# Kernel tuning notes

Measured on AMD Instinct MI355X. Metric: run time of the kernel, lower is better.

Reference implementation:

```python
import jax, jax.numpy as jnp
import numpy as np

B, HGT, WID, D, NS = 4, 64, 128, 128, 2
LN_EPS = 1e-5

def layer_norm(x, g, b):
    m = jnp.mean(x, axis=-1, keepdims=True)
    v = jnp.mean((x - m) ** 2, axis=-1, keepdims=True)
    return (x - m) * jax.lax.rsqrt(v + LN_EPS) * g + b

def setup_inputs() -> dict:
    key = jax.random.key(0)
    ks = jax.random.split(key, 8)
    src = jax.random.normal(ks[0], (B, HGT * WID, D), jnp.float32)
    L = (HGT // NS) * (WID // NS)  # 2048
    s = 0.05
    return {
        "source": src,
        "target": src,  # identical -> self-attention branch in original
        "shifted_window_attn_mask": jax.random.normal(ks[1], (NS * NS, L, L), jnp.float32),
        "shifted_window_attn_mask_1d": jnp.zeros((NS, WID // NS, WID // NS), jnp.float32),
        "height": HGT,
        "width": WID,
        "attn_num_splits": NS,
        "with_shift": 1,
        "Wq": jax.random.normal(ks[2], (D, D), jnp.float32) * s,
        "Wk": jax.random.normal(ks[3], (D, D), jnp.float32) * s,
        "Wv": jax.random.normal(ks[4], (D, D), jnp.float32) * s,
        "Wm": jax.random.normal(ks[5], (D, D), jnp.float32) * s,
        "g1": jnp.ones((D,), jnp.float32),
        "b1": jnp.zeros((D,), jnp.float32),
        "W1": jax.random.normal(ks[6], (2 * D, 8 * D), jnp.float32) * s,
        "W2": jax.random.normal(ks[7], (8 * D, D), jnp.float32) * s,
        "g2": jnp.ones((D,), jnp.float32),
        "b2": jnp.zeros((D,), jnp.float32),
    }

def _shifted_window_self_attn(q, k, v, ns, with_shift, h, w, attn_mask):
    b, _, c = q.shape
    hh, ww = h // ns, w // ns  # window sizes
    sh, sw = hh // 2, ww // 2
    L = hh * ww

    def to_windows(x):
        x = x.reshape(b, h, w, c)
        if with_shift:
            x = jnp.roll(x, shift=(-sh, -sw), axis=(1, 2))
        # (b, ns, hh, ns, ww, c) -> (b*ns*ns, hh*ww, c)
        x = x.reshape(b, ns, hh, ns, ww, c).transpose(0, 1, 3, 2, 4, 5)
        return x.reshape(b * ns * ns, L, c)

    qw, kw, vw = to_windows(q), to_windows(k), to_windows(v)
    scores = jnp.einsum("bqc,bkc->bqk", qw, kw) / (c ** 0.5)  # (b*ns^2, L, L)
    if with_shift:
        scores = (scores.reshape(b, ns * ns, L, L) + attn_mask).reshape(b * ns * ns, L, L)
    attn = jax.nn.softmax(scores, axis=-1)
    out = jnp.einsum("bqk,bkc->bqc", attn, vw)
    # merge windows back
    out = out.reshape(b, ns, ns, hh, ww, c).transpose(0, 1, 3, 2, 4, 5).reshape(b, h, w, c)
    if with_shift:
        out = jnp.roll(out, shift=(sh, sw), axis=(1, 2))
    return out.reshape(b, h * w, c)

def reference(source, target, shifted_window_attn_mask, shifted_window_attn_mask_1d,
              height, width, attn_num_splits, with_shift,
              Wq, Wk, Wv, Wm, g1, b1, W1, W2, g2, b2):
    # target == source -> self-attention, attn_num_splits > 1 -> shifted-window path
    q = source @ Wq
    k = target @ Wk
    v = target @ Wv
    message = _shifted_window_self_attn(q, k, v, attn_num_splits, with_shift,
                                        height, width, shifted_window_attn_mask)
    message = layer_norm(message @ Wm, g1, b1)
    h = jnp.concatenate([source, message], axis=-1)  # (B, HW, 2D)
    message = jax.nn.gelu(h @ W1, approximate=False) @ W2
    message = layer_norm(message, g2, b2)
    return source + message
```

## Files before the change

kernel.cpp:

```cpp
#include <hip/hip_runtime.h>

typedef unsigned short u16;
typedef __bf16 bf16x8 __attribute__((ext_vector_type(8)));
typedef float f32x4 __attribute__((ext_vector_type(4)));

#define MFMA(a, b, c) __builtin_amdgcn_mfma_f32_16x16x32_bf16(a, b, c, 0, 0, 0)


__device__ __forceinline__ u16 f2b(float f) {
  unsigned u = __builtin_bit_cast(unsigned, f);
  u += 0x7fffu + ((u >> 16) & 1u);
  return (u16)(u >> 16);
}
__device__ __forceinline__ float b2f(u16 h) {
  unsigned u = (unsigned)h << 16;
  return __builtin_bit_cast(float, u);
}
__device__ __forceinline__ void glds16(const u16* g, u16* l) {
  __builtin_amdgcn_global_load_lds((const __attribute__((address_space(1))) void*)g,
                                   (__attribute__((address_space(3))) void*)l, 16, 0, 0);
}

#define QW_OFF   ((size_t)0)
#define KW_OFF   ((size_t)8 << 20)
#define VBUF_OFF ((size_t)16 << 20)
#define O1_OFF   ((size_t)24 << 20)
#define O2_OFF   ((size_t)40 << 20)
#define HID_OFF  ((size_t)0)
#define SRCB_OFF ((size_t)64 << 20)
#define MSG1_OFF ((size_t)72 << 20)
#define L1_OFF   ((size_t)80 << 20)
#define L2P_OFF  (((size_t)80 << 20) + 131072)
#define WQT_OFF  (((size_t)80 << 20) + 262144)
#define WKT_OFF  (WQT_OFF + 32768)
#define WVT_OFF  (WQT_OFF + 65536)
#define WMT_OFF  (WQT_OFF + 98304)
#define W1T_OFF  (WQT_OFF + 131072)
#define W2T_OFF  (WQT_OFF + 655360)

__global__ void k_prep(const float* __restrict__ wq, const float* __restrict__ wk,
                       const float* __restrict__ wv, const float* __restrict__ wm,
                       const float* __restrict__ w1, const float* __restrict__ w2,
                       u16* __restrict__ wqt, u16* __restrict__ wkt,
                       u16* __restrict__ wvt, u16* __restrict__ wmt,
                       u16* __restrict__ w1t, u16* __restrict__ w2t) {
  int t = blockIdx.x * 256 + threadIdx.x;
  if (t < 65536) {
    int m = t >> 14, loc = t & 16383;
    int n = loc >> 7, k = loc & 127;
    const float* s = (m == 0) ? wq : (m == 1) ? wk : (m == 2) ? wv : wm;
    u16* d = (m == 0) ? wqt : (m == 1) ? wkt : (m == 2) ? wvt : wmt;
    const float sc = (m == 0) ? 0.08838834764831845f : 1.0f;
    d[n * 128 + k] = f2b(s[k * 128 + n] * sc);
  } else if (t < 65536 + 262144) {
    int loc = t - 65536;
    int n = loc >> 8, k = loc & 255;
    w1t[n * 256 + k] = f2b(w1[k * 1024 + n]);
  } else if (t < 65536 + 262144 + 131072) {
    int loc = t - 327680;
    int n = loc >> 10, k = loc & 1023;
    w2t[n * 1024 + k] = f2b(w2[k * 128 + n]);
  }
}

__global__ __launch_bounds__(256, 2)
void k_qkv(const float* __restrict__ src,
           const u16* __restrict__ wtq, const u16* __restrict__ wtk,
           const u16* __restrict__ wtv,
           u16* __restrict__ qw, u16* __restrict__ kw, u16* __restrict__ vbuf,
           u16* __restrict__ srcb) {
  __shared__ __align__(16) u16 At[64 * 136];
  __shared__ __align__(16) u16 Bt[128 * 136];
  const int tid = threadIdx.x, bid = blockIdx.x;
  const int lane = tid & 63, wid = tid >> 6;
  const int l15 = lane & 15, quad = lane >> 4;

  {
    const int row = tid >> 2, part = tid & 3;
    const int t = bid * 64 + row;
    const int g = t >> 11, p = t & 2047;
    const int b = g >> 2, wi = (g >> 1) & 1, wj = g & 1;
    const int ii = p >> 6, jj = p & 63;
    const int y = (wi * 32 + ii + 16) & 63;
    const int x = (wj * 64 + jj + 32) & 127;
    const int srow = b * 8192 + y * 128 + x;
    const float4* sp = (const float4*)(src + srow * 128) + part * 8;
    u16* lp = &At[row * 136 + part * 32];
    u16* gp = srcb + srow * 128 + part * 32;
#pragma unroll
    for (int q = 0; q < 8; ++q) {
      float4 v = sp[q];
      ushort4 h = make_ushort4(f2b(v.x), f2b(v.y), f2b(v.z), f2b(v.w));
      *(ushort4*)(lp + q * 4) = h;
      *(ushort4*)(gp + q * 4) = h;
    }
  }
  __syncthreads();

  bf16x8 afrag[4];
  const int arow = wid * 16 + l15;
#pragma unroll
  for (int kk = 0; kk < 4; ++kk)
    afrag[kk] = *(const bf16x8*)&At[arow * 136 + kk * 32 + quad * 8];

  const f32x4 fz = {0.f, 0.f, 0.f, 0.f};
#pragma unroll 1
  for (int m = 0; m < 3; ++m) {
    const u16* wp = (m == 0) ? wtq : (m == 1) ? wtk : wtv;
    {
      const int n = tid >> 1, half = tid & 1;
      const uint4* sp = (const uint4*)(wp + n * 128 + half * 64);
      uint4* dp = (uint4*)&Bt[n * 136 + half * 64];
#pragma unroll
      for (int q = 0; q < 8; ++q) dp[q] = sp[q];
    }
    __syncthreads();
    f32x4 acc[8];
#pragma unroll
    for (int nt = 0; nt < 8; ++nt) acc[nt] = fz;
#pragma unroll
    for (int kk = 0; kk < 4; ++kk) {
#pragma unroll
      for (int nt = 0; nt < 8; ++nt) {
        bf16x8 bfr = *(const bf16x8*)&Bt[(nt * 16 + l15) * 136 + kk * 32 + quad * 8];
        acc[nt] = MFMA(afrag[kk], bfr, acc[nt]);
      }
    }
    const int t0 = bid * 64 + wid * 16 + quad * 4;
    if (m < 2) {
      u16* dst = (m == 0) ? qw : kw;
#pragma unroll
      for (int nt = 0; nt < 8; ++nt) {
        const int d = nt * 16 + l15;
#pragma unroll
        for (int r = 0; r < 4; ++r) dst[(t0 + r) * 128 + d] = f2b(acc[nt][r]);
      }
    } else {
      const int g = bid >> 5;
      const int p0 = t0 & 2047;
#pragma unroll
      for (int nt = 0; nt < 8; ++nt) {
        const int d = nt * 16 + l15;
        ushort4 hv = make_ushort4(f2b(acc[nt][0]), f2b(acc[nt][1]),
                                  f2b(acc[nt][2]), f2b(acc[nt][3]));
        *(ushort4*)&vbuf[g * 262144 + d * 2048 + p0] = hv;
      }
    }
    __syncthreads();
  }
}

__global__ __launch_bounds__(256, 4)
void k_attn(const u16* __restrict__ qw, const u16* __restrict__ kw,
            const u16* __restrict__ vbuf, const float* __restrict__ mask,
            u16* __restrict__ o1, u16* __restrict__ o2,
            float* __restrict__ l1, float* __restrict__ l2) {
  __shared__ __align__(16) u16 Kt[2][32 * 128];
  __shared__ __align__(16) u16 Vt[2][128 * 32];
  __shared__ __align__(16) u16 Pt[64 * 40];
  const int tid = threadIdx.x, bid = blockIdx.x;
  const int lane = tid & 63, wid = tid >> 6;
  const int l15 = lane & 15, quad = lane >> 4;
  const int b = bid & 3, w = (bid >> 2) & 3, half = (bid >> 4) & 1, qb = bid >> 5;
  const int g = b * 4 + w;
  const int k0 = half * 1024;
  const u16* kbase = kw + g * 262144 + k0 * 128;
  const u16* vbase = vbuf + g * 262144 + k0;
  const int qrow0 = qb * 64 + wid * 16 + quad * 4;
  const float* mlane = mask + (size_t)w * 4194304 + (size_t)qrow0 * 2048 + k0 + l15;

  int offk[2], offv[2], dstb[2];
#pragma unroll
  for (int j = 0; j < 2; ++j) {
    const int s = wid * 128 + j * 64 + lane;
    const int rk = s >> 4, bk = (s & 15) ^ (rk & 15);
    offk[j] = rk * 128 + bk * 8;
    const int dv = s >> 2, bv = (s & 3) ^ (dv & 3);
    offv[j] = dv * 2048 + bv * 8;
    dstb[j] = (wid * 128 + j * 64) * 8;
  }

  bf16x8 qfrag[4];
  {
    const u16* qp = qw + g * 262144 + (qb * 64 + wid * 16 + l15) * 128 + quad * 8;
#pragma unroll
    for (int kk = 0; kk < 4; ++kk) qfrag[kk] = *(const bf16x8*)(qp + kk * 32);
  }
  const f32x4 fz = {0.f, 0.f, 0.f, 0.f};
  f32x4 o[8];
#pragma unroll
  for (int nt = 0; nt < 8; ++nt) o[nt] = fz;
  float lr[4] = {0.f, 0.f, 0.f, 0.f};
  const float L2E = 1.4426950408889634f;

#pragma unroll
  for (int j = 0; j < 2; ++j) {
    glds16(kbase + offk[j], &Kt[0][dstb[j]]);
    glds16(vbase + offv[j], &Vt[0][dstb[j]]);
  }
  float mpf[8];
#pragma unroll
  for (int nt = 0; nt < 2; ++nt)
#pragma unroll
    for (int r = 0; r < 4; ++r) mpf[nt * 4 + r] = mlane[r * 2048 + nt * 16];

#pragma unroll 1
  for (int kt = 0; kt < 32; ++kt) {
    const int p = kt & 1;
    __syncthreads();
    if (kt < 31) {
      const u16* kb = kbase + (kt + 1) * 4096;
      const u16* vb = vbase + (kt + 1) * 32;
#pragma unroll
      for (int j = 0; j < 2; ++j) {
        glds16(kb + offk[j], &Kt[p ^ 1][dstb[j]]);
        glds16(vb + offv[j], &Vt[p ^ 1][dstb[j]]);
      }
    }
    float mn[8];
    if (kt < 31) {
#pragma unroll
      for (int nt = 0; nt < 2; ++nt)
#pragma unroll
        for (int r = 0; r < 4; ++r)
          mn[nt * 4 + r] = mlane[r * 2048 + (kt + 1) * 32 + nt * 16];
    }

    f32x4 s[2];
#pragma unroll
    for (int nt = 0; nt < 2; ++nt)
#pragma unroll
      for (int r = 0; r < 4; ++r) s[nt][r] = mpf[nt * 4 + r];
#pragma unroll
    for (int kk = 0; kk < 4; ++kk)
#pragma unroll
      for (int nt = 0; nt < 2; ++nt) {
        bf16x8 bfr = *(const bf16x8*)&Kt[p][(nt * 16 + l15) * 128 +
                                           (((kk * 4 + quad) ^ l15) * 8)];
        s[nt] = MFMA(qfrag[kk], bfr, s[nt]);
      }
#pragma unroll
    for (int nt = 0; nt < 2; ++nt)
#pragma unroll
      for (int r = 0; r < 4; ++r) {
        const float pv = exp2f(s[nt][r] * L2E);
        lr[r] += pv;
        Pt[(wid * 16 + quad * 4 + r) * 40 + nt * 16 + l15] = f2b(pv);
      }
    bf16x8 pfrag = *(const bf16x8*)&Pt[(wid * 16 + l15) * 40 + quad * 8];
#pragma unroll
    for (int nt = 0; nt < 8; ++nt) {
      bf16x8 bfr = *(const bf16x8*)&Vt[p][(nt * 16 + l15) * 32 +
                                          ((quad ^ (l15 & 3)) * 8)];
      o[nt] = MFMA(pfrag, bfr, o[nt]);
    }
    if (kt < 31) {
#pragma unroll
      for (int i = 0; i < 8; ++i) mpf[i] = mn[i];
    }
  }

#pragma unroll
  for (int off = 1; off < 16; off <<= 1)
#pragma unroll
    for (int r = 0; r < 4; ++r) lr[r] += __shfl_xor(lr[r], off, 16);
  u16* op = half ? o2 : o1;
  float* lp = half ? l2 : l1;
  const int t0 = g * 2048 + qrow0;
#pragma unroll
  for (int r = 0; r < 4; ++r) {
    const float inv = 1.f / lr[r];
#pragma unroll
    for (int nt = 0; nt < 8; ++nt)
      op[(size_t)(t0 + r) * 128 + nt * 16 + l15] = f2b(o[nt][r] * inv);
    if (l15 == 0) lp[t0 + r] = lr[r];
  }
}

__global__ __launch_bounds__(256, 2)
void k_wmln(const u16* __restrict__ o1, const u16* __restrict__ o2,
            const float* __restrict__ l1, const float* __restrict__ l2,
            const u16* __restrict__ wmt, const float* __restrict__ g1,
            const float* __restrict__ b1, u16* __restrict__ msg1) {
  __shared__ __align__(16) u16 At[64 * 136];
  __shared__ __align__(16) u16 Bt[128 * 136];
  const int tid = threadIdx.x, bid = blockIdx.x;
  const int lane = tid & 63, wid = tid >> 6;
  const int l15 = lane & 15, quad = lane >> 4;
  {
    const int row = tid >> 2, part = tid & 3;
    const int m = bid * 64 + row;
    const float la = l1[m], lb = l2[m];
    const float wA = la / (la + lb), wB = lb / (la + lb);
    const u16* p1 = o1 + (size_t)m * 128 + part * 32;
    const u16* p2 = o2 + (size_t)m * 128 + part * 32;
    u16* lp = &At[row * 136 + part * 32];
#pragma unroll
    for (int q = 0; q < 4; ++q) {
      ushort4 xa = *(const ushort4*)(p1 + q * 8);
      ushort4 xb = *(const ushort4*)(p1 + q * 8 + 4);
      ushort4 ya = *(const ushort4*)(p2 + q * 8);
      ushort4 yb = *(const ushort4*)(p2 + q * 8 + 4);
      ushort4 ha = make_ushort4(f2b(b2f(xa.x) * wA + b2f(ya.x) * wB),
                                f2b(b2f(xa.y) * wA + b2f(ya.y) * wB),
                                f2b(b2f(xa.z) * wA + b2f(ya.z) * wB),
                                f2b(b2f(xa.w) * wA + b2f(ya.w) * wB));
      ushort4 hb = make_ushort4(f2b(b2f(xb.x) * wA + b2f(yb.x) * wB),
                                f2b(b2f(xb.y) * wA + b2f(yb.y) * wB),
                                f2b(b2f(xb.z) * wA + b2f(yb.z) * wB),
                                f2b(b2f(xb.w) * wA + b2f(yb.w) * wB));
      *(ushort4*)(lp + q * 8) = ha;
      *(ushort4*)(lp + q * 8 + 4) = hb;
    }
  }
  {
    const int n = tid >> 1, half = tid & 1;
    const uint4* sp = (const uint4*)(wmt + n * 128 + half * 64);
    uint4* dp = (uint4*)&Bt[n * 136 + half * 64];
#pragma unroll
    for (int q = 0; q < 8; ++q) dp[q] = sp[q];
  }
  __syncthreads();
  bf16x8 afrag[4];
  const int arow = wid * 16 + l15;
#pragma unroll
  for (int kk = 0; kk < 4; ++kk)
    afrag[kk] = *(const bf16x8*)&At[arow * 136 + kk * 32 + quad * 8];
  const f32x4 fz = {0.f, 0.f, 0.f, 0.f};
  f32x4 acc[8];
#pragma unroll
  for (int nt = 0; nt < 8; ++nt) acc[nt] = fz;
#pragma unroll
  for (int kk = 0; kk < 4; ++kk)
#pragma unroll
    for (int nt = 0; nt < 8; ++nt) {
      bf16x8 bfr = *(const bf16x8*)&Bt[(nt * 16 + l15) * 136 + kk * 32 + quad * 8];
      acc[nt] = MFMA(afrag[kk], bfr, acc[nt]);
    }
  float sum[4] = {0, 0, 0, 0}, sq[4] = {0, 0, 0, 0};
#pragma unroll
  for (int nt = 0; nt < 8; ++nt)
#pragma unroll
    for (int r = 0; r < 4; ++r) {
      const float v = acc[nt][r];
      sum[r] += v;
      sq[r] += v * v;
    }
#pragma unroll
  for (int off = 1; off < 16; off <<= 1)
#pragma unroll
    for (int r = 0; r < 4; ++r) {
      sum[r] += __shfl_xor(sum[r], off, 16);
      sq[r] += __shfl_xor(sq[r], off, 16);
    }
  float mean[4], rstd[4];
#pragma unroll
  for (int r = 0; r < 4; ++r) {
    mean[r] = sum[r] * (1.f / 128.f);
    const float var = sq[r] * (1.f / 128.f) - mean[r] * mean[r];
    rstd[r] = rsqrtf(var + 1e-5f);
  }
  const int t0 = bid * 64 + wid * 16 + quad * 4;
#pragma unroll
  for (int nt = 0; nt < 8; ++nt) {
    const int d = nt * 16 + l15;
    const float gg = g1[d], bb = b1[d];
#pragma unroll
    for (int r = 0; r < 4; ++r) {
      const int tt = t0 + r;
      const int gw = tt >> 11, pp = tt & 2047;
      const int bb2 = gw >> 2, wi = (gw >> 1) & 1, wj = gw & 1;
      const int ii = pp >> 6, jj = pp & 63;
      const int yy = (wi * 32 + ii + 16) & 63;
      const int xx = (wj * 64 + jj + 32) & 127;
      msg1[(bb2 * 8192 + yy * 128 + xx) * 128 + d] =
          f2b((acc[nt][r] - mean[r]) * rstd[r] * gg + bb);
    }
  }
}

__global__ __launch_bounds__(256, 3)
void k_mlp1(const u16* __restrict__ srcb, const u16* __restrict__ msg1,
            const u16* __restrict__ w1t, u16* __restrict__ hid) {
  __shared__ __align__(16) u16 At[64 * 72];
  __shared__ __align__(16) u16 Bt[256 * 72];
  const int tid = threadIdx.x, bid = blockIdx.x;
  const int rb = bid >> 2, nb = bid & 3;
  const int lane = tid & 63, wid = tid >> 6;
  const int l15 = lane & 15, quad = lane >> 4;
  const f32x4 fz = {0.f, 0.f, 0.f, 0.f};
  f32x4 acc[16];
#pragma unroll
  for (int nt = 0; nt < 16; ++nt) acc[nt] = fz;
#pragma unroll 1
  for (int kc = 0; kc < 4; ++kc) {
    __syncthreads();
    {
      const int row = tid >> 2, part = tid & 3;
      const u16* sp0 = (kc < 2) ? srcb : msg1;
      const uint4* sp = (const uint4*)(sp0 + (rb * 64 + row) * 128 + (kc & 1) * 64 + part * 16);
      uint4* dp = (uint4*)&At[row * 72 + part * 16];
      dp[0] = sp[0];
      dp[1] = sp[1];
    }
    {
      const uint4* sp = (const uint4*)(w1t + (nb * 256 + tid) * 256 + kc * 64);
      uint4* dp = (uint4*)&Bt[tid * 72];
#pragma unroll
      for (int q = 0; q < 8; ++q) dp[q] = sp[q];
    }
    __syncthreads();
#pragma unroll
    for (int kk = 0; kk < 2; ++kk) {
      bf16x8 a = *(const bf16x8*)&At[(wid * 16 + l15) * 72 + kk * 32 + quad * 8];
#pragma unroll
      for (int nt = 0; nt < 16; ++nt) {
        bf16x8 b = *(const bf16x8*)&Bt[(nt * 16 + l15) * 72 + kk * 32 + quad * 8];
        acc[nt] = MFMA(a, b, acc[nt]);
      }
    }
  }
  const int t0 = rb * 64 + wid * 16 + quad * 4;
#pragma unroll
  for (int nt = 0; nt < 16; ++nt) {
    const int n = nb * 256 + nt * 16 + l15;
#pragma unroll
    for (int r = 0; r < 4; ++r) {
      const float x = acc[nt][r];
      const float y = 0.5f * x * (1.f + erff(x * 0.70710678118654752f));
      hid[(size_t)(t0 + r) * 1024 + n] = f2b(y);
    }
  }
}

__global__ __launch_bounds__(256, 2)
void k_mlp2(const u16* __restrict__ hid, const u16* __restrict__ w2t,
            const float* __restrict__ g2, const float* __restrict__ b2,
            const float* __restrict__ src, float* __restrict__ out) {
  __shared__ __align__(16) u16 At[64 * 72];
  __shared__ __align__(16) u16 Bt[128 * 72];
  const int tid = threadIdx.x, bid = blockIdx.x;
  const int lane = tid & 63, wid = tid >> 6;
  const int l15 = lane & 15, quad = lane >> 4;
  const f32x4 fz = {0.f, 0.f, 0.f, 0.f};
  f32x4 acc[8];
#pragma unroll
  for (int nt = 0; nt < 8; ++nt) acc[nt] = fz;
#pragma unroll 1
  for (int kc = 0; kc < 16; ++kc) {
    __syncthreads();
    {
      const int row = tid >> 2, part = tid & 3;
      const uint4* sp = (const uint4*)(hid + (size_t)(bid * 64 + row) * 1024 + kc * 64 + part * 16);
      uint4* dp = (uint4*)&At[row * 72 + part * 16];
      dp[0] = sp[0];
      dp[1] = sp[1];
    }
    {
      const int n = tid >> 1, half = tid & 1;
      const uint4* sp = (const uint4*)(w2t + n * 1024 + kc * 64 + half * 32);
      uint4* dp = (uint4*)&Bt[n * 72 + half * 32];
#pragma unroll
      for (int q = 0; q < 4; ++q) dp[q] = sp[q];
    }
    __syncthreads();
#pragma unroll
    for (int kk = 0; kk < 2; ++kk) {
      bf16x8 a = *(const bf16x8*)&At[(wid * 16 + l15) * 72 + kk * 32 + quad * 8];
#pragma unroll
      for (int nt = 0; nt < 8; ++nt) {
        bf16x8 b = *(const bf16x8*)&Bt[(nt * 16 + l15) * 72 + kk * 32 + quad * 8];
        acc[nt] = MFMA(a, b, acc[nt]);
      }
    }
  }
  float sum[4] = {0, 0, 0, 0}, sq[4] = {0, 0, 0, 0};
#pragma unroll
  for (int nt = 0; nt < 8; ++nt)
#pragma unroll
    for (int r = 0; r < 4; ++r) {
      const float v = acc[nt][r];
      sum[r] += v;
      sq[r] += v * v;
    }
#pragma unroll
  for (int off = 1; off < 16; off <<= 1)
#pragma unroll
    for (int r = 0; r < 4; ++r) {
      sum[r] += __shfl_xor(sum[r], off, 16);
      sq[r] += __shfl_xor(sq[r], off, 16);
    }
  float mean[4], rstd[4];
#pragma unroll
  for (int r = 0; r < 4; ++r) {
    mean[r] = sum[r] * (1.f / 128.f);
    const float var = sq[r] * (1.f / 128.f) - mean[r] * mean[r];
    rstd[r] = rsqrtf(var + 1e-5f);
  }
  const int t0 = bid * 64 + wid * 16 + quad * 4;
#pragma unroll
  for (int nt = 0; nt < 8; ++nt) {
    const int d = nt * 16 + l15;
    const float gg = g2[d], bb = b2[d];
#pragma unroll
    for (int r = 0; r < 4; ++r) {
      const int idx = (t0 + r) * 128 + d;
      out[idx] = src[idx] + (acc[nt][r] - mean[r]) * rstd[r] * gg + bb;
    }
  }
}

extern "C" void kernel_launch(void* const* d_in, const int* in_sizes, int n_in,
                              void* d_out, int out_size, void* d_ws, size_t ws_size,
                              hipStream_t stream) {
  const float* src  = (const float*)d_in[0];
  const float* mask = (const float*)d_in[2];
  const float* Wq = (const float*)d_in[8];
  const float* Wk = (const float*)d_in[9];
  const float* Wv = (const float*)d_in[10];
  const float* Wm = (const float*)d_in[11];
  const float* g1 = (const float*)d_in[12];
  const float* b1 = (const float*)d_in[13];
  const float* W1 = (const float*)d_in[14];
  const float* W2 = (const float*)d_in[15];
  const float* g2 = (const float*)d_in[16];
  const float* b2 = (const float*)d_in[17];
  char* ws = (char*)d_ws;
  u16* qw   = (u16*)(ws + QW_OFF);
  u16* kw   = (u16*)(ws + KW_OFF);
  u16* vbuf = (u16*)(ws + VBUF_OFF);
  u16* o1   = (u16*)(ws + O1_OFF);
  u16* o2   = (u16*)(ws + O2_OFF);
  float* l1 = (float*)(ws + L1_OFF);
  float* l2 = (float*)(ws + L2P_OFF);
  u16* hid  = (u16*)(ws + HID_OFF);
  u16* srcb = (u16*)(ws + SRCB_OFF);
  u16* msg1 = (u16*)(ws + MSG1_OFF);
  u16* wqt = (u16*)(ws + WQT_OFF);
  u16* wkt = (u16*)(ws + WKT_OFF);
  u16* wvt = (u16*)(ws + WVT_OFF);
  u16* wmt = (u16*)(ws + WMT_OFF);
  u16* w1t = (u16*)(ws + W1T_OFF);
  u16* w2t = (u16*)(ws + W2T_OFF);

  k_prep<<<1792, 256, 0, stream>>>(Wq, Wk, Wv, Wm, W1, W2, wqt, wkt, wvt, wmt, w1t, w2t);
  k_qkv<<<512, 256, 0, stream>>>(src, wqt, wkt, wvt, qw, kw, vbuf, srcb);
  k_attn<<<1024, 256, 0, stream>>>(qw, kw, vbuf, mask, o1, o2, l1, l2);
  k_wmln<<<512, 256, 0, stream>>>(o1, o2, l1, l2, wmt, g1, b1, msg1);
  k_mlp1<<<2048, 256, 0, stream>>>(srcb, msg1, w1t, hid);
  k_mlp2<<<512, 256, 0, stream>>>(hid, w2t, g2, b2, src, (float*)d_out);
}
```

Before: 332.5 us.

## Double attention tile per block: 128 query rows, 64-key tiles, remapped grid

Each k_attn block now covers 128 query rows, with 32 rows (two 16-row MFMA subtiles) per wave, and loads 64-key K/V tiles per iteration instead of 32. Each K/V fragment read from LDS therefore feeds two MFMAs, the number of barriers is halved, and the grid shrinks from 1024 to 512 blocks. Block indices are also permuted so that consecutive blocks map to different windows and halves. In exchange, register and LDS use per block go up, occupancy drops (launch bounds go from 4 to 2), and the grid has fewer blocks to spread across the CUs.

```diff
diff --git a/kernel.cpp b/kernel.cpp
--- a/kernel.cpp
+++ b/kernel.cpp
@@ -150,15 +150,16 @@
   }
 }
 
-__global__ __launch_bounds__(256, 4)
+__global__ __launch_bounds__(256, 2)
 void k_attn(const u16* __restrict__ qw, const u16* __restrict__ kw,
             const u16* __restrict__ vbuf, const float* __restrict__ mask,
             u16* __restrict__ o1, u16* __restrict__ o2,
             float* __restrict__ l1, float* __restrict__ l2) {
-  __shared__ __align__(16) u16 Kt[2][32 * 128];
-  __shared__ __align__(16) u16 Vt[2][128 * 32];
-  __shared__ __align__(16) u16 Pt[64 * 40];
-  const int tid = threadIdx.x, bid = blockIdx.x;
+  __shared__ __align__(16) u16 Kt[2][64 * 128];
+  __shared__ __align__(16) u16 Vt[2][128 * 64];
+  __shared__ __align__(16) u16 Pt[128 * 40];
+  const int tid = threadIdx.x;
+  const int bid = (blockIdx.x & 7) * 64 + (blockIdx.x >> 3);
   const int lane = tid & 63, wid = tid >> 6;
   const int l15 = lane & 15, quad = lane >> 4;
   const int b = bid & 3, w = (bid >> 2) & 3, half = (bid >> 4) & 1, qb = bid >> 5;
@@ -166,114 +167,138 @@
   const int k0 = half * 1024;
   const u16* kbase = kw + g * 262144 + k0 * 128;
   const u16* vbase = vbuf + g * 262144 + k0;
-  const int qrow0 = qb * 64 + wid * 16 + quad * 4;
-  const float* mlane = mask + (size_t)w * 4194304 + (size_t)qrow0 * 2048 + k0 + l15;
-
-  int offk[2], offv[2], dstb[2];
-#pragma unroll
-  for (int j = 0; j < 2; ++j) {
-    const int s = wid * 128 + j * 64 + lane;
+  const int qrow0 = qb * 128 + wid * 32;
+  const float* mlane = mask + (size_t)w * 4194304 + (size_t)(qrow0 + quad * 4) * 2048 + k0 + l15;
+
+  int offk[4], offv[4], dstb[4];
+#pragma unroll
+  for (int j = 0; j < 4; ++j) {
+    const int s = wid * 256 + j * 64 + lane;
     const int rk = s >> 4, bk = (s & 15) ^ (rk & 15);
     offk[j] = rk * 128 + bk * 8;
-    const int dv = s >> 2, bv = (s & 3) ^ (dv & 3);
+    const int dv = s >> 3, bv = (s & 7) ^ (dv & 7);
     offv[j] = dv * 2048 + bv * 8;
-    dstb[j] = (wid * 128 + j * 64) * 8;
-  }
-
-  bf16x8 qfrag[4];
-  {
-    const u16* qp = qw + g * 262144 + (qb * 64 + wid * 16 + l15) * 128 + quad * 8;
-#pragma unroll
-    for (int kk = 0; kk < 4; ++kk) qfrag[kk] = *(const bf16x8*)(qp + kk * 32);
+    dstb[j] = (wid * 256 + j * 64) * 8;
+  }
+
+  bf16x8 qfrag[2][4];
+#pragma unroll
+  for (int qs = 0; qs < 2; ++qs) {
+    const u16* qp = qw + g * 262144 + (qrow0 + qs * 16 + l15) * 128 + quad * 8;
+#pragma unroll
+    for (int kk = 0; kk < 4; ++kk) qfrag[qs][kk] = *(const bf16x8*)(qp + kk * 32);
   }
   const f32x4 fz = {0.f, 0.f, 0.f, 0.f};
-  f32x4 o[8];
-#pragma unroll
-  for (int nt = 0; nt < 8; ++nt) o[nt] = fz;
-  float lr[4] = {0.f, 0.f, 0.f, 0.f};
+  f32x4 o[2][8];
+#pragma unroll
+  for (int qs = 0; qs < 2; ++qs)
+#pragma unroll
+    for (int nt = 0; nt < 8; ++nt) o[qs][nt] = fz;
+  float lr[2][4] = {{0.f, 0.f, 0.f, 0.f}, {0.f, 0.f, 0.f, 0.f}};
   const float L2E = 1.4426950408889634f;
 
 #pragma unroll
-  for (int j = 0; j < 2; ++j) {
+  for (int j = 0; j < 4; ++j) {
     glds16(kbase + offk[j], &Kt[0][dstb[j]]);
     glds16(vbase + offv[j], &Vt[0][dstb[j]]);
   }
-  float mpf[8];
-#pragma unroll
-  for (int nt = 0; nt < 2; ++nt)
-#pragma unroll
-    for (int r = 0; r < 4; ++r) mpf[nt * 4 + r] = mlane[r * 2048 + nt * 16];
+  float mpf[16];
+#pragma unroll
+  for (int qs = 0; qs < 2; ++qs)
+#pragma unroll
+    for (int ntl = 0; ntl < 2; ++ntl)
+#pragma unroll
+      for (int r = 0; r < 4; ++r)
+        mpf[qs * 8 + ntl * 4 + r] = mlane[(qs * 16 + r) * 2048 + ntl * 16];
 
 #pragma unroll 1
-  for (int kt = 0; kt < 32; ++kt) {
+  for (int kt = 0; kt < 16; ++kt) {
     const int p = kt & 1;
     __syncthreads();
-    if (kt < 31) {
-      const u16* kb = kbase + (kt + 1) * 4096;
-      const u16* vb = vbase + (kt + 1) * 32;
-#pragma unroll
-      for (int j = 0; j < 2; ++j) {
+    if (kt < 15) {
+      const u16* kb = kbase + (kt + 1) * 8192;
+      const u16* vb = vbase + (kt + 1) * 64;
+#pragma unroll
+      for (int j = 0; j < 4; ++j) {
         glds16(kb + offk[j], &Kt[p ^ 1][dstb[j]]);
         glds16(vb + offv[j], &Vt[p ^ 1][dstb[j]]);
       }
     }
-    float mn[8];
-    if (kt < 31) {
-#pragma unroll
-      for (int nt = 0; nt < 2; ++nt)
-#pragma unroll
-        for (int r = 0; r < 4; ++r)
-          mn[nt * 4 + r] = mlane[r * 2048 + (kt + 1) * 32 + nt * 16];
-    }
-
-    f32x4 s[2];
-#pragma unroll
-    for (int nt = 0; nt < 2; ++nt)
-#pragma unroll
-      for (int r = 0; r < 4; ++r) s[nt][r] = mpf[nt * 4 + r];
-#pragma unroll
-    for (int kk = 0; kk < 4; ++kk)
-#pragma unroll
-      for (int nt = 0; nt < 2; ++nt) {
-        bf16x8 bfr = *(const bf16x8*)&Kt[p][(nt * 16 + l15) * 128 +
-                                           (((kk * 4 + quad) ^ l15) * 8)];
-        s[nt] = MFMA(qfrag[kk], bfr, s[nt]);
-      }
-#pragma unroll
-    for (int nt = 0; nt < 2; ++nt)
-#pragma unroll
-      for (int r = 0; r < 4; ++r) {
-        const float pv = exp2f(s[nt][r] * L2E);
-        lr[r] += pv;
-        Pt[(wid * 16 + quad * 4 + r) * 40 + nt * 16 + l15] = f2b(pv);
-      }
-    bf16x8 pfrag = *(const bf16x8*)&Pt[(wid * 16 + l15) * 40 + quad * 8];
-#pragma unroll
-    for (int nt = 0; nt < 8; ++nt) {
-      bf16x8 bfr = *(const bf16x8*)&Vt[p][(nt * 16 + l15) * 32 +
-                                          ((quad ^ (l15 & 3)) * 8)];
-      o[nt] = MFMA(pfrag, bfr, o[nt]);
-    }
-    if (kt < 31) {
-#pragma unroll
-      for (int i = 0; i < 8; ++i) mpf[i] = mn[i];
+#pragma unroll
+    for (int ks = 0; ks < 2; ++ks) {
+      float mn[16];
+      const bool hasn = (kt < 15) || (ks == 0);
+      const int ncol = kt * 64 + 32 + ks * 32;
+      if (hasn) {
+#pragma unroll
+        for (int qs = 0; qs < 2; ++qs)
+#pragma unroll
+          for (int ntl = 0; ntl < 2; ++ntl)
+#pragma unroll
+            for (int r = 0; r < 4; ++r)
+              mn[qs * 8 + ntl * 4 + r] = mlane[(qs * 16 + r) * 2048 + ncol + ntl * 16];
+      }
+      f32x4 s[2][2];
+#pragma unroll
+      for (int qs = 0; qs < 2; ++qs)
+#pragma unroll
+        for (int ntl = 0; ntl < 2; ++ntl)
+#pragma unroll
+          for (int r = 0; r < 4; ++r) s[qs][ntl][r] = mpf[qs * 8 + ntl * 4 + r];
+#pragma unroll
+      for (int kk = 0; kk < 4; ++kk)
+#pragma unroll
+        for (int ntl = 0; ntl < 2; ++ntl) {
+          bf16x8 kfr = *(const bf16x8*)&Kt[p][(ks * 32 + ntl * 16 + l15) * 128 +
+                                             (((kk * 4 + quad) ^ l15) * 8)];
+          s[0][ntl] = MFMA(qfrag[0][kk], kfr, s[0][ntl]);
+          s[1][ntl] = MFMA(qfrag[1][kk], kfr, s[1][ntl]);
+        }
+#pragma unroll
+      for (int qs = 0; qs < 2; ++qs)
+#pragma unroll
+        for (int ntl = 0; ntl < 2; ++ntl)
+#pragma unroll
+          for (int r = 0; r < 4; ++r) {
+            const float pv = exp2f(s[qs][ntl][r] * L2E);
+            lr[qs][r] += pv;
+            Pt[(wid * 32 + qs * 16 + quad * 4 + r) * 40 + ntl * 16 + l15] = f2b(pv);
+          }
+      bf16x8 pf0 = *(const bf16x8*)&Pt[(wid * 32 + l15) * 40 + quad * 8];
+      bf16x8 pf1 = *(const bf16x8*)&Pt[(wid * 32 + 16 + l15) * 40 + quad * 8];
+#pragma unroll
+      for (int nt = 0; nt < 8; ++nt) {
+        bf16x8 vfr = *(const bf16x8*)&Vt[p][(nt * 16 + l15) * 64 +
+                                            (((ks * 4 + quad) ^ (l15 & 7)) * 8)];
+        o[0][nt] = MFMA(pf0, vfr, o[0][nt]);
+        o[1][nt] = MFMA(pf1, vfr, o[1][nt]);
+      }
+      if (hasn) {
+#pragma unroll
+        for (int i = 0; i < 16; ++i) mpf[i] = mn[i];
+      }
     }
   }
 
 #pragma unroll
   for (int off = 1; off < 16; off <<= 1)
 #pragma unroll
-    for (int r = 0; r < 4; ++r) lr[r] += __shfl_xor(lr[r], off, 16);
+    for (int qs = 0; qs < 2; ++qs)
+#pragma unroll
+      for (int r = 0; r < 4; ++r) lr[qs][r] += __shfl_xor(lr[qs][r], off, 16);
   u16* op = half ? o2 : o1;
   float* lp = half ? l2 : l1;
-  const int t0 = g * 2048 + qrow0;
-#pragma unroll
-  for (int r = 0; r < 4; ++r) {
-    const float inv = 1.f / lr[r];
-#pragma unroll
-    for (int nt = 0; nt < 8; ++nt)
-      op[(size_t)(t0 + r) * 128 + nt * 16 + l15] = f2b(o[nt][r] * inv);
-    if (l15 == 0) lp[t0 + r] = lr[r];
+#pragma unroll
+  for (int qs = 0; qs < 2; ++qs) {
+    const int t0 = g * 2048 + qrow0 + qs * 16 + quad * 4;
+#pragma unroll
+    for (int r = 0; r < 4; ++r) {
+      const float inv = 1.f / lr[qs][r];
+#pragma unroll
+      for (int nt = 0; nt < 8; ++nt)
+        op[(size_t)(t0 + r) * 128 + nt * 16 + l15] = f2b(o[qs][nt][r] * inv);
+      if (l15 == 0) lp[t0 + r] = lr[qs][r];
+    }
   }
 }
 
@@ -545,7 +570,7 @@
 
   k_prep<<<1792, 256, 0, stream>>>(Wq, Wk, Wv, Wm, W1, W2, wqt, wkt, wvt, wmt, w1t, w2t);
   k_qkv<<<512, 256, 0, stream>>>(src, wqt, wkt, wvt, qw, kw, vbuf, srcb);
-  k_attn<<<1024, 256, 0, stream>>>(qw, kw, vbuf, mask, o1, o2, l1, l2);
+  k_attn<<<512, 256, 0, stream>>>(qw, kw, vbuf, mask, o1, o2, l1, l2);
   k_wmln<<<512, 256, 0, stream>>>(o1, o2, l1, l2, wmt, g1, b1, msg1);
   k_mlp1<<<2048, 256, 0, stream>>>(srcb, msg1, w1t, hid);
   k_mlp2<<<512, 256, 0, stream>>>(hid, w2t, g2, b2, src, (float*)d_out);
```

After: 323.0 us. -2.9%, faster.
